# Kernel tuning notes

Hardware: AMD Instinct MI355X
Metric: run time of the kernel (lower is better)

## Reference

```python
import jax, jax.numpy as jnp
import numpy as np

B, L, A, D = 16, 1024, 512, 1024


def setup_inputs() -> dict:
    key = jax.random.key(0)
    ks = jax.random.split(key, 12)
    s = 1.0 / np.sqrt(D)
    s2 = 1.0 / np.sqrt(2 * D)
    return {
        "text_features": jax.random.normal(ks[0], (B, L, D), jnp.float32),
        "audio_features": jax.random.normal(ks[1], (B, A, D), jnp.float32),
        "Wt1": jax.random.uniform(ks[2], (D, D), jnp.float32, -s, s),
        "bt1": jax.random.uniform(ks[3], (D,), jnp.float32, -s, s),
        "Wa1": jax.random.uniform(ks[4], (D, D), jnp.float32, -s, s),
        "w_att1": jax.random.uniform(ks[5], (2 * D,), jnp.float32, -s2, s2),
        "b_att1": jax.random.uniform(ks[6], (), jnp.float32, -s2, s2),
        "Wt2": jax.random.uniform(ks[7], (D, D), jnp.float32, -s, s),
        "Wa2": jax.random.uniform(ks[8], (D, D), jnp.float32, -s, s),
        "ba2": jax.random.uniform(ks[9], (D,), jnp.float32, -s, s),
        "w_att2": jax.random.uniform(ks[10], (2 * D,), jnp.float32, -s2, s2),
        "b_att2": jax.random.uniform(ks[11], (), jnp.float32, -s2, s2),
    }


def reference(text_features, audio_features, Wt1, bt1, Wa1, w_att1, b_att1,
              Wt2, Wa2, ba2, w_att2, b_att2):
    # Additive co-attention. tanh(cat([u_i, v_j])) = cat([tanh(u_i), tanh(v_j)]),
    # so the post-tanh linear score decomposes into an outer sum — exact same math
    # as the naive repeat/cat/tanh/linear, without the (B,L,A,2D) intermediate.
    d = Wt1.shape[0]
    # --- attention over audio regions ---
    u1 = jnp.tanh(jnp.einsum('bld,ed->ble', text_features, Wt1) + bt1)   # (B,L,D)
    v1 = jnp.tanh(jnp.einsum('bad,ed->bae', audio_features, Wa1))        # (B,A,D)
    scores1 = (u1 @ w_att1[:d])[:, :, None] + (v1 @ w_att1[d:])[:, None, :] + b_att1  # (B,L,A)
    audio_att = jax.nn.softmax(scores1, axis=-1)
    att_audio_features = jnp.einsum('bla,bad->bld', audio_att, audio_features)  # (B,L,D)
    # --- attention over text positions (self.args.max_seq_len == L) ---
    u2 = jnp.tanh(jnp.einsum('bld,ed->ble', att_audio_features, Wa2) + ba2)  # (B,L,D)
    v2 = jnp.tanh(jnp.einsum('bkd,ed->bke', text_features, Wt2))             # (B,L,D)
    scores2 = (u2 @ w_att2[:d])[:, :, None] + (v2 @ w_att2[d:])[:, None, :] + b_att2  # (B,L,L)
    textual_att = jax.nn.softmax(scores2, axis=-1)
    att_text_features = jnp.einsum('blk,bkd->bld', textual_att, text_features)
    return (att_text_features, att_audio_features)
```

## Files before the change

kernel.cpp:

```cpp
#include <hip/hip_runtime.h>

typedef unsigned short u16;
typedef float f32x4 __attribute__((ext_vector_type(4)));
typedef int   i32x4 __attribute__((ext_vector_type(4)));
typedef u16   u16x8 __attribute__((ext_vector_type(8)));

#define SWZ(i) ((i) ^ ((((i) >> 6) & 3) << 3))

__device__ __forceinline__ u16 f2bf(float f) {
  unsigned u = __float_as_uint(f);
  u += 0x7FFFu + ((u >> 16) & 1u);
  return (u16)(u >> 16);
}

__device__ __forceinline__ float tanh_fast(float x) {
  float e = __expf(2.0f * x);
  return 1.0f - 2.0f / (e + 1.0f);
}

__device__ __forceinline__ void mfma_bf16(f32x4& acc, i32x4 a, i32x4 b) {
  asm("v_mfma_f32_16x16x32_bf16 %0, %1, %2, %0" : "+v"(acc) : "v"(a), "v"(b));
}

__global__ __launch_bounds__(256) void cast_all_kernel(
    const float* __restrict__ text, const float* __restrict__ audio,
    const float* __restrict__ w2, const float* __restrict__ w1,
    u16* __restrict__ tb, u16* __restrict__ ab,
    u16* __restrict__ w2b, u16* __restrict__ w1b) {
  const int NTOT = 3407872;
  int stride = gridDim.x * 256;
  for (int i = blockIdx.x * 256 + threadIdx.x; i < NTOT; i += stride) {
    const float* src; u16* dst; int j;
    if (i < 2097152)      { src = text;  dst = tb;  j = i; }
    else if (i < 3145728) { src = audio; dst = ab;  j = i - 2097152; }
    else if (i < 3276800) { src = w2;    dst = w2b; j = i - 3145728; }
    else                  { src = w1;    dst = w1b; j = i - 3276800; }
    const float4* s = (const float4*)src;
    float4 a = s[2 * j], b = s[2 * j + 1];
    u16x8 o;
    o[0] = f2bf(a.x); o[1] = f2bf(a.y); o[2] = f2bf(a.z); o[3] = f2bf(a.w);
    o[4] = f2bf(b.x); o[5] = f2bf(b.y); o[6] = f2bf(b.z); o[7] = f2bf(b.w);
    *(u16x8*)(dst + (size_t)8 * j) = o;
  }
}

__global__ __launch_bounds__(512, 4) void score_kernel(
    const u16* __restrict__ Xa, const u16* __restrict__ Wa,
    const float* __restrict__ wva, float* __restrict__ sva,
    const u16* __restrict__ Xt, const u16* __restrict__ Wt,
    const float* __restrict__ wvt, float* __restrict__ svt) {
  __shared__ u16 At[2][4096];
  __shared__ u16 Bt[2][8192];

  int bx = blockIdx.x;
  const u16 *X, *W; const float* wv; float* svout; int mt, split, M;
  if (bx < 256) {
    X = Xa; W = Wa; wv = wva; svout = sva; M = 8192;
    mt = (bx >> 5) * 8 + (bx & 7); split = (bx >> 3) & 3;
  } else {
    int x = bx - 256;
    X = Xt; W = Wt; wv = wvt; svout = svt; M = 16384;
    mt = (x >> 5) * 8 + (x & 7); split = (x >> 3) & 3;
  }
  const int n0 = split * 256;

  const int t = threadIdx.x;
  const int wid = t >> 6, lane = t & 63;
  const int wm = wid >> 2, wn = wid & 3;
  const int lane15 = lane & 15, lg = lane >> 4;

  const int sr = t >> 2, sc = (t & 3) * 8;
  const int wiA  = SWZ(sr * 32 + sc);
  const int wiB1 = SWZ((128 + sr) * 32 + sc);

  const u16* Xb = X + (size_t)mt * 128 * 1024;
  const u16* Wp = W + (size_t)n0 * 1024;

  f32x4 acc[4][4];
  #pragma unroll
  for (int mi = 0; mi < 4; ++mi)
    #pragma unroll
    for (int ni = 0; ni < 4; ++ni)
      acc[mi][ni] = (f32x4){0.f, 0.f, 0.f, 0.f};

  i32x4 ra  = *(const i32x4*)(Xb + (size_t)sr * 1024 + sc);
  i32x4 rb0 = *(const i32x4*)(Wp + (size_t)sr * 1024 + sc);
  i32x4 rb1 = *(const i32x4*)(Wp + (size_t)(128 + sr) * 1024 + sc);
  *(i32x4*)(At[0] + wiA)  = ra;
  *(i32x4*)(Bt[0] + wiA)  = rb0;
  *(i32x4*)(Bt[0] + wiB1) = rb1;
  __syncthreads();

  for (int kt = 0; kt < 32; ++kt) {
    const int cur = kt & 1;
    if (kt < 31) {
      const int k1 = (kt + 1) * 32;
      ra  = *(const i32x4*)(Xb + (size_t)sr * 1024 + k1 + sc);
      rb0 = *(const i32x4*)(Wp + (size_t)sr * 1024 + k1 + sc);
      rb1 = *(const i32x4*)(Wp + (size_t)(128 + sr) * 1024 + k1 + sc);
    }
    i32x4 af[4], bfr[4];
    #pragma unroll
    for (int mi = 0; mi < 4; ++mi) {
      int rr = wm * 64 + mi * 16 + lane15;
      af[mi] = *(const i32x4*)(At[cur] + SWZ(rr * 32 + lg * 8));
    }
    #pragma unroll
    for (int ni = 0; ni < 4; ++ni) {
      int rr = wn * 64 + ni * 16 + lane15;
      bfr[ni] = *(const i32x4*)(Bt[cur] + SWZ(rr * 32 + lg * 8));
    }
    #pragma unroll
    for (int mi = 0; mi < 4; ++mi)
      #pragma unroll
      for (int ni = 0; ni < 4; ++ni)
        mfma_bf16(acc[mi][ni], af[mi], bfr[ni]);
    if (kt < 31) {
      *(i32x4*)(At[cur ^ 1] + wiA)  = ra;
      *(i32x4*)(Bt[cur ^ 1] + wiA)  = rb0;
      *(i32x4*)(Bt[cur ^ 1] + wiB1) = rb1;
    }
    __syncthreads();
  }

  float wvn[4];
  #pragma unroll
  for (int ni = 0; ni < 4; ++ni) wvn[ni] = wv[n0 + wn * 64 + ni * 16 + lane15];
  float rs[4][4];
  #pragma unroll
  for (int mi = 0; mi < 4; ++mi)
    #pragma unroll
    for (int r = 0; r < 4; ++r) {
      float v = 0.f;
      #pragma unroll
      for (int ni = 0; ni < 4; ++ni)
        v += tanh_fast(acc[mi][ni][r]) * wvn[ni];
      rs[mi][r] = v;
    }

  float* sred = (float*)At;
  #pragma unroll
  for (int mi = 0; mi < 4; ++mi)
    #pragma unroll
    for (int r = 0; r < 4; ++r) {
      float v = rs[mi][r];
      v += __shfl_xor(v, 1);
      v += __shfl_xor(v, 2);
      v += __shfl_xor(v, 4);
      v += __shfl_xor(v, 8);
      if (lane15 == 0)
        sred[wn * 128 + wm * 64 + mi * 16 + lg * 4 + r] = v;
    }
  __syncthreads();
  if (t < 128)
    svout[(size_t)split * M + (size_t)mt * 128 + t] =
        sred[t] + sred[128 + t] + sred[256 + t] + sred[384 + t];
}

__global__ __launch_bounds__(256) void softq_bcast_kernel(
    const float* __restrict__ xA, const float* __restrict__ svA,
    const float* __restrict__ xT, const float* __restrict__ svT,
    float* __restrict__ out) {
  int bx = blockIdx.x;
  int stage = bx >> 8;
  int b = (bx >> 4) & 15, dch = bx & 15;
  int Acnt = stage ? 1024 : 512;
  int M = stage ? 16384 : 8192;
  const float* x = stage ? xT : xA;
  const float* svp = stage ? svT : svA;
  int rowbase = b * Acnt;

  __shared__ float p[1024];
  __shared__ float red[256];
  __shared__ float chunk[64];
  int t = threadIdx.x;

  float mloc = -1e30f;
  for (int a = t; a < Acnt; a += 256) {
    float v = svp[rowbase + a] + svp[M + rowbase + a] +
              svp[2 * M + rowbase + a] + svp[3 * M + rowbase + a];
    p[a] = v;
    mloc = fmaxf(mloc, v);
  }
  #pragma unroll
  for (int off = 32; off; off >>= 1) mloc = fmaxf(mloc, __shfl_xor(mloc, off));
  if ((t & 63) == 0) red[t >> 6] = mloc;
  __syncthreads();
  float mx = fmaxf(fmaxf(red[0], red[1]), fmaxf(red[2], red[3]));

  float sloc = 0.f;
  for (int a = t; a < Acnt; a += 256) {
    float e = __expf(p[a] - mx);
    p[a] = e;
    sloc += e;
  }
  #pragma unroll
  for (int off = 32; off; off >>= 1) sloc += __shfl_xor(sloc, off);
  __syncthreads();
  if ((t & 63) == 0) red[t >> 6] = sloc;
  __syncthreads();
  float inv = 1.0f / (red[0] + red[1] + red[2] + red[3]);

  int dl = t & 63, ag = t >> 6;
  const float* xb = x + (size_t)rowbase * 1024 + dch * 64 + dl;
  float acc = 0.f;
  #pragma unroll 8
  for (int a = ag; a < Acnt; a += 4) acc += p[a] * xb[(size_t)a * 1024];
  __syncthreads();
  red[t] = acc;
  __syncthreads();
  if (t < 64) {
    float tot = red[t] + red[t + 64] + red[t + 128] + red[t + 192];
    chunk[t] = tot * inv;
  }
  __syncthreads();

  size_t base4 = ((stage ? (size_t)0 : (size_t)16777216) +
                  (size_t)b * 1048576 + (size_t)dch * 64) >> 2;
  f32x4* o4 = (f32x4*)out;
  f32x4 v = ((f32x4*)chunk)[t & 15];
  int q = t & 15;
  #pragma unroll 4
  for (int l = t >> 4; l < 1024; l += 16)
    __builtin_nontemporal_store(v, &o4[base4 + (size_t)l * 256 + q]);
}

extern "C" void kernel_launch(void* const* d_in, const int* in_sizes, int n_in,
                              void* d_out, int out_size, void* d_ws, size_t ws_size,
                              hipStream_t stream) {
  const float* text  = (const float*)d_in[0];
  const float* audio = (const float*)d_in[1];
  const float* Wa1   = (const float*)d_in[4];
  const float* watt1 = (const float*)d_in[5];
  const float* Wt2   = (const float*)d_in[7];
  const float* watt2 = (const float*)d_in[10];

  char* ws = (char*)d_ws;
  u16*   tb  = (u16*)(ws);
  u16*   ab  = (u16*)(ws + 33554432);
  u16*   w2b = (u16*)(ws + 50331648);
  u16*   w1b = (u16*)(ws + 52428800);
  float* sv2 = (float*)(ws + 54525952);
  float* sv1 = (float*)(ws + 54788096);

  cast_all_kernel<<<2048, 256, 0, stream>>>(text, audio, Wt2, Wa1,
                                            tb, ab, w2b, w1b);

  score_kernel<<<768, 512, 0, stream>>>(ab, w1b, watt1 + 1024, sv1,
                                        tb, w2b, watt2 + 1024, sv2);

  softq_bcast_kernel<<<512, 256, 0, stream>>>(audio, sv1, text, sv2,
                                              (float*)d_out);
}
```

Measured before the change: 323.7 us.

## Use direct global-to-LDS loads in score GEMM and bf16 inputs for weighted sum

The score GEMM now stages A and B tiles with global_load_lds (direct to LDS), with the swizzle moved into the source column index, so tiles no longer pass through registers and separate LDS stores. The softmax-weighted reduction reads the bf16-cast copies of text and audio instead of the fp32 originals, halving that read traffic. The risks are reduced precision in the attended features, since fp32 inputs are replaced by bf16, and a possible sync hazard, because async LDS loads are covered only by the plain barrier.

```diff
diff --git a/kernel.cpp b/kernel.cpp
--- a/kernel.cpp
+++ b/kernel.cpp
@@ -20,6 +20,12 @@
 
 __device__ __forceinline__ void mfma_bf16(f32x4& acc, i32x4 a, i32x4 b) {
   asm("v_mfma_f32_16x16x32_bf16 %0, %1, %2, %0" : "+v"(acc) : "v"(a), "v"(b));
+}
+
+__device__ __forceinline__ void gload16(const u16* g, u16* l) {
+  __builtin_amdgcn_global_load_lds(
+      (const __attribute__((address_space(1))) void*)g,
+      (__attribute__((address_space(3))) void*)l, 16, 0, 0);
 }
 
 __global__ __launch_bounds__(256) void cast_all_kernel(
@@ -69,13 +75,16 @@
   const int wm = wid >> 2, wn = wid & 3;
   const int lane15 = lane & 15, lg = lane >> 4;
 
-  const int sr = t >> 2, sc = (t & 3) * 8;
-  const int wiA  = SWZ(sr * 32 + sc);
-  const int wiB1 = SWZ((128 + sr) * 32 + sc);
-
   const u16* Xb = X + (size_t)mt * 128 * 1024;
   const u16* Wp = W + (size_t)n0 * 1024;
 
+  const int srow = wid * 16 + (lane >> 2);
+  const int scol = (((lane & 3) ^ ((lane >> 3) & 3)) << 3);
+  const u16* gA  = Xb + (size_t)srow * 1024 + scol;
+  const u16* gB0 = Wp + (size_t)srow * 1024 + scol;
+  const u16* gB1 = Wp + (size_t)(128 + srow) * 1024 + scol;
+  const int lofs = wid * 512 + lane * 8;
+
   f32x4 acc[4][4];
   #pragma unroll
   for (int mi = 0; mi < 4; ++mi)
@@ -83,21 +92,18 @@
     for (int ni = 0; ni < 4; ++ni)
       acc[mi][ni] = (f32x4){0.f, 0.f, 0.f, 0.f};
 
-  i32x4 ra  = *(const i32x4*)(Xb + (size_t)sr * 1024 + sc);
-  i32x4 rb0 = *(const i32x4*)(Wp + (size_t)sr * 1024 + sc);
-  i32x4 rb1 = *(const i32x4*)(Wp + (size_t)(128 + sr) * 1024 + sc);
-  *(i32x4*)(At[0] + wiA)  = ra;
-  *(i32x4*)(Bt[0] + wiA)  = rb0;
-  *(i32x4*)(Bt[0] + wiB1) = rb1;
+  gload16(gA,  At[0] + lofs);
+  gload16(gB0, Bt[0] + lofs);
+  gload16(gB1, Bt[0] + 4096 + lofs);
   __syncthreads();
 
   for (int kt = 0; kt < 32; ++kt) {
     const int cur = kt & 1;
     if (kt < 31) {
       const int k1 = (kt + 1) * 32;
-      ra  = *(const i32x4*)(Xb + (size_t)sr * 1024 + k1 + sc);
-      rb0 = *(const i32x4*)(Wp + (size_t)sr * 1024 + k1 + sc);
-      rb1 = *(const i32x4*)(Wp + (size_t)(128 + sr) * 1024 + k1 + sc);
+      gload16(gA + k1,  At[cur ^ 1] + lofs);
+      gload16(gB0 + k1, Bt[cur ^ 1] + lofs);
+      gload16(gB1 + k1, Bt[cur ^ 1] + 4096 + lofs);
     }
     i32x4 af[4], bfr[4];
     #pragma unroll
@@ -115,11 +121,6 @@
       #pragma unroll
       for (int ni = 0; ni < 4; ++ni)
         mfma_bf16(acc[mi][ni], af[mi], bfr[ni]);
-    if (kt < 31) {
-      *(i32x4*)(At[cur ^ 1] + wiA)  = ra;
-      *(i32x4*)(Bt[cur ^ 1] + wiA)  = rb0;
-      *(i32x4*)(Bt[cur ^ 1] + wiB1) = rb1;
-    }
     __syncthreads();
   }
 
@@ -158,15 +159,15 @@
 }
 
 __global__ __launch_bounds__(256) void softq_bcast_kernel(
-    const float* __restrict__ xA, const float* __restrict__ svA,
-    const float* __restrict__ xT, const float* __restrict__ svT,
+    const u16* __restrict__ xA, const float* __restrict__ svA,
+    const u16* __restrict__ xT, const float* __restrict__ svT,
     float* __restrict__ out) {
   int bx = blockIdx.x;
   int stage = bx >> 8;
   int b = (bx >> 4) & 15, dch = bx & 15;
   int Acnt = stage ? 1024 : 512;
   int M = stage ? 16384 : 8192;
-  const float* x = stage ? xT : xA;
+  const u16* x = stage ? xT : xA;
   const float* svp = stage ? svT : svA;
   int rowbase = b * Acnt;
 
@@ -202,10 +203,11 @@
   float inv = 1.0f / (red[0] + red[1] + red[2] + red[3]);
 
   int dl = t & 63, ag = t >> 6;
-  const float* xb = x + (size_t)rowbase * 1024 + dch * 64 + dl;
+  const u16* xb = x + (size_t)rowbase * 1024 + dch * 64 + dl;
   float acc = 0.f;
   #pragma unroll 8
-  for (int a = ag; a < Acnt; a += 4) acc += p[a] * xb[(size_t)a * 1024];
+  for (int a = ag; a < Acnt; a += 4)
+    acc += p[a] * __uint_as_float(((unsigned)xb[(size_t)a * 1024]) << 16);
   __syncthreads();
   red[t] = acc;
   __syncthreads();
@@ -249,6 +251,6 @@
   score_kernel<<<768, 512, 0, stream>>>(ab, w1b, watt1 + 1024, sv1,
                                         tb, w2b, watt2 + 1024, sv2);
 
-  softq_bcast_kernel<<<512, 256, 0, stream>>>(audio, sv1, text, sv2,
+  softq_bcast_kernel<<<512, 256, 0, stream>>>(ab, sv1, tb, sv2,
                                               (float*)d_out);
 }
```

Result: no change. 325.1 us (+0.4%).
